# Kernel tuning notes

Measured on AMD Instinct MI355X. Metric: run time of the kernel, lower is better.

The kernel has to match this reference:

```python
import jax, jax.numpy as jnp
import numpy as np

T = 0.1  # temperature (init arg t)


def setup_inputs() -> dict:
    key = jax.random.key(0)
    k0, k1, k2, k3 = jax.random.split(key, 4)
    B, C, H, W, N = 1, 64, 256, 256, 4096
    emb_0 = jax.random.normal(k0, (B, C, H, W), dtype=jnp.float32)
    emb_1 = jax.random.normal(k1, (B, C, H, W), dtype=jnp.float32)
    # module assumes embeddings are already L2-normalized along channels
    emb_0 = emb_0 / jnp.linalg.norm(emb_0, axis=1, keepdims=True)
    emb_1 = emb_1 / jnp.linalg.norm(emb_1, axis=1, keepdims=True)
    locations_0 = jax.random.randint(k2, (B, N, 2), 0, H).astype(jnp.float32)
    locations_1 = jax.random.randint(k3, (B, N, 2), 0, H).astype(jnp.float32)
    return {"emb_0": emb_0, "emb_1": emb_1,
            "locations_0": locations_0, "locations_1": locations_1}


def reference(emb_0, emb_1, locations_0, locations_1):
    b, c, H, W = emb_0.shape  # b == 1
    n = locations_0.shape[1]
    v = H * W
    # (b, v, c)
    e0 = emb_0.reshape(b, c, v).transpose(0, 2, 1)
    e1 = emb_1.reshape(b, c, v).transpose(0, 2, 1)
    # flatten 2D coords to linear indices: strides [W, 1]
    ind_kernel = jnp.array([W, 1], dtype=jnp.float32)
    ind_0 = (jnp.floor(locations_0) @ ind_kernel).astype(jnp.int32)[0]  # (n,)
    ind_1 = (jnp.floor(locations_1) @ ind_kernel).astype(jnp.int32)[0]  # (n,)
    e0 = e0[:, ind_0, :]  # (b, n, c)
    e1 = e1[:, ind_1, :]  # (b, n, c)
    emb = jnp.concatenate([e0, e1], axis=1)  # (b, 2n, c)
    sim = jnp.einsum('bic,bjc->bij', emb, emb)  # (b, 2n, 2n)
    exp = jnp.exp(sim / T)
    sum_e = jnp.sum(exp, axis=2) - np.exp(1.0 / T)  # subtract self-similarity
    u = jnp.arange(n)
    w = u + n
    e_uv = exp[:, u, w]  # (b, n) positive pairs
    loss = -jnp.sum(jnp.log(e_uv / sum_e[:, u]) + jnp.log(e_uv / sum_e[:, w]))
    return loss / (2 * n)
```

## Files before the change

kernel.cpp:

```cpp
#include <hip/hip_runtime.h>
#include <math.h>

#define HW2     65536
#define NLOC    4096
#define NROW    8192
#define CDIM    64
#define TINV    10.0f
#define EXP10   22026.465794806718f
#define NP      64
#define NPAIR   2080

#if __has_builtin(__builtin_amdgcn_exp2f)
#define ASCALE  14.426950408889634f
#define EXPFN(x) __builtin_amdgcn_exp2f(x)
#else
#define ASCALE  10.0f
#define EXPFN(x) __expf(x)
#endif

typedef __attribute__((ext_vector_type(8))) short bf16x8;
typedef __attribute__((ext_vector_type(4))) float f32x4;
typedef unsigned short u16;

__device__ __forceinline__ unsigned short f2bf(float f) {
  unsigned u = __builtin_bit_cast(unsigned, f);
  u += 0x7FFFu + ((u >> 16) & 1u);
  return (unsigned short)(u >> 16);
}
__device__ __forceinline__ float bf2f(unsigned u16v) {
  unsigned u = u16v << 16;
  return __builtin_bit_cast(float, u);
}

__global__ __launch_bounds__(256) void transpose_kernel(
    const float* __restrict__ emb0, const float* __restrict__ emb1,
    u16* __restrict__ embT0, u16* __restrict__ embT1) {
  __shared__ u16 T[64 * 72];
  const int tid = threadIdx.x;
  const float* emb = blockIdx.y ? emb1 : emb0;
  u16* embT        = blockIdx.y ? embT1 : embT0;
  const int w0 = blockIdx.x * 64;

#pragma unroll
  for (int q = 0; q < 4; ++q) {
    const int c = q * 16 + (tid >> 4);
    const int x = tid & 15;
    float4 v = *reinterpret_cast<const float4*>(&emb[(size_t)c * HW2 + w0 + x * 4]);
    T[(x * 4 + 0) * 72 + c] = f2bf(v.x);
    T[(x * 4 + 1) * 72 + c] = f2bf(v.y);
    T[(x * 4 + 2) * 72 + c] = f2bf(v.z);
    T[(x * 4 + 3) * 72 + c] = f2bf(v.w);
  }
  __syncthreads();
#pragma unroll
  for (int q = 0; q < 2; ++q) {
    const int w  = q * 32 + (tid >> 3);
    const int c8 = tid & 7;
    bf16x8 v = *reinterpret_cast<const bf16x8*>(&T[w * 72 + c8 * 8]);
    *reinterpret_cast<bf16x8*>(&embT[(size_t)(w0 + w) * CDIM + c8 * 8]) = v;
  }
}

__global__ __launch_bounds__(256) void gather2_kernel(
    const u16* __restrict__ embT0, const u16* __restrict__ embT1,
    const float* __restrict__ loc0, const float* __restrict__ loc1,
    u16* __restrict__ Ga, u16* __restrict__ Gb) {
  const int t = blockIdx.x * 256 + threadIdx.x;
  const int i = t >> 3;
  const int p = t & 7;
  const float* loc = (i < NLOC) ? loc0 : loc1;
  const u16*   eT  = (i < NLOC) ? embT0 : embT1;
  const int u = (i < NLOC) ? i : i - NLOC;
  const int ind = (int)floorf(loc[u * 2]) * 256 + (int)floorf(loc[u * 2 + 1]);
  bf16x8 v = *reinterpret_cast<const bf16x8*>(&eT[(size_t)ind * CDIM + p * 8]);
  *reinterpret_cast<bf16x8*>(&Gb[(size_t)i * CDIM + p * 8]) = v;
  bf16x8 vs;
#pragma unroll
  for (int e = 0; e < 8; ++e) {
    float f = bf2f((unsigned short)v[e]);
    vs[e] = (short)f2bf(f * ASCALE);
  }
  *reinterpret_cast<bf16x8*>(&Ga[(size_t)i * CDIM + p * 8]) = vs;
}

__global__ __launch_bounds__(256) void gather_kernel(
    const float* __restrict__ emb0, const float* __restrict__ emb1,
    const float* __restrict__ loc0, const float* __restrict__ loc1,
    u16* __restrict__ Ga, u16* __restrict__ Gb) {
  int t = blockIdx.x * 256 + threadIdx.x;
  int i = t >> 6;
  int c = t & 63;
  const float* loc = (i < NLOC) ? loc0 : loc1;
  const float* emb = (i < NLOC) ? emb0 : emb1;
  int u = (i < NLOC) ? i : (i - NLOC);
  int ind = (int)floorf(loc[u * 2]) * 256 + (int)floorf(loc[u * 2 + 1]);
  float v = emb[(size_t)c * HW2 + ind];
  Gb[t] = f2bf(v);
  Ga[t] = f2bf(v * ASCALE);
}

__device__ __forceinline__ void stage_tile(u16* Bs, const u16* __restrict__ Gb,
                                           int jb, int buf, int tid, int wave,
                                           int srow, int ssl) {
#pragma unroll
  for (int r = 0; r < 2; ++r) {
    const u16* src = Gb + (size_t)(jb + r * 32 + srow) * CDIM + ssl * 8;
#if __has_builtin(__builtin_amdgcn_global_load_lds)
    u16* dst = Bs + buf * 4096 + r * 2048 + wave * 512;
    __builtin_amdgcn_global_load_lds(
        (const __attribute__((address_space(1))) unsigned int*)src,
        (__attribute__((address_space(3))) unsigned int*)dst, 16, 0, 0);
#else
    bf16x8 tmp = *reinterpret_cast<const bf16x8*>(src);
    *reinterpret_cast<bf16x8*>(Bs + buf * 4096 + r * 2048 + tid * 8) = tmp;
#endif
  }
}

__global__ __launch_bounds__(256) void simsum_tri_kernel(
    const u16* __restrict__ Ga, const u16* __restrict__ Gb,
    float* __restrict__ rowPart) {
  __shared__ u16 Bs[2 * 64 * CDIM];
  __shared__ float colRed[4][128];

  const int tid  = threadIdx.x;
  const int lane = tid & 63;
  const int wave = tid >> 6;
  const int lrow = lane & 15;
  const int kh   = lane >> 4;

  const int b = blockIdx.x;
  int p = (int)((129.0f - sqrtf(16641.0f - 8.0f * (float)b)) * 0.5f);
  if (p < 0) p = 0;
  if (p > NP - 1) p = NP - 1;
#pragma unroll
  for (int it = 0; it < 3; ++it) {
    if (p > 0 && (p * NP - p * (p - 1) / 2) > b) --p;
    else if (((p + 1) * NP - (p + 1) * p / 2) <= b) ++p;
  }
  const int q  = p + (b - (p * NP - p * (p - 1) / 2));
  const int p0 = p * 128, q0 = q * 128;
  const int i0 = p0 + wave * 32;

  const bf16x8* arowA =
      reinterpret_cast<const bf16x8*>(Ga + (size_t)(i0 + lrow) * CDIM + kh * 8);
  const bf16x8* arowB =
      reinterpret_cast<const bf16x8*>(Ga + (size_t)(i0 + 16 + lrow) * CDIM + kh * 8);
  bf16x8 aA0 = arowA[0], aA1 = arowA[4];
  bf16x8 aB0 = arowB[0], aB1 = arowB[4];

  const int srow = tid >> 3;
  const int ssl  = (tid & 7) ^ (srow & 7);
  stage_tile(Bs, Gb, q0,      0, tid, wave, srow, ssl);
  stage_tile(Bs, Gb, q0 + 64, 1, tid, wave, srow, ssl);
  __syncthreads();

  const int sp0 = ((kh ^ (lrow & 7)) << 3);
  const int sp1 = (((4 + kh) ^ (lrow & 7)) << 3);

  float accA[4][4], accB[4][4];
#pragma unroll
  for (int nf = 0; nf < 4; ++nf)
#pragma unroll
    for (int r = 0; r < 4; ++r) { accA[nf][r] = 0.f; accB[nf][r] = 0.f; }
  float colAcc[2][4];

#pragma unroll
  for (int t = 0; t < 2; ++t) {
    const u16* bs = Bs + t * 4096;
#pragma unroll
    for (int nf = 0; nf < 4; ++nf) {
      const int rb = (nf * 16 + lrow) * CDIM;
      bf16x8 b0 = *reinterpret_cast<const bf16x8*>(bs + rb + sp0);
      bf16x8 b1 = *reinterpret_cast<const bf16x8*>(bs + rb + sp1);
      f32x4 z = {0.f, 0.f, 0.f, 0.f};
      f32x4 tA = __builtin_amdgcn_mfma_f32_16x16x32_bf16(aA0, b0, z, 0, 0, 0);
      tA = __builtin_amdgcn_mfma_f32_16x16x32_bf16(aA1, b1, tA, 0, 0, 0);
      f32x4 tB = __builtin_amdgcn_mfma_f32_16x16x32_bf16(aB0, b0, z, 0, 0, 0);
      tB = __builtin_amdgcn_mfma_f32_16x16x32_bf16(aB1, b1, tB, 0, 0, 0);
      float cp = 0.f;
#pragma unroll
      for (int r = 0; r < 4; ++r) {
        float eA = EXPFN(tA[r]);
        float eB = EXPFN(tB[r]);
        accA[nf][r] += eA;
        accB[nf][r] += eB;
        cp += eA + eB;
      }
      colAcc[t][nf] = cp;
    }
  }

#pragma unroll
  for (int r = 0; r < 4; ++r) {
    float vA = (accA[0][r] + accA[1][r]) + (accA[2][r] + accA[3][r]);
    float vB = (accB[0][r] + accB[1][r]) + (accB[2][r] + accB[3][r]);
    vA += __shfl_xor(vA, 1, 16);
    vA += __shfl_xor(vA, 2, 16);
    vA += __shfl_xor(vA, 4, 16);
    vA += __shfl_xor(vA, 8, 16);
    vB += __shfl_xor(vB, 1, 16);
    vB += __shfl_xor(vB, 2, 16);
    vB += __shfl_xor(vB, 4, 16);
    vB += __shfl_xor(vB, 8, 16);
    if (lrow == 0) {
      rowPart[(size_t)(i0 + kh * 4 + r) * NP + q] = vA;
      rowPart[(size_t)(i0 + 16 + kh * 4 + r) * NP + q] = vB;
    }
  }

  if (p != q) {
#pragma unroll
    for (int t = 0; t < 2; ++t)
#pragma unroll
      for (int nf = 0; nf < 4; ++nf) {
        float c = colAcc[t][nf];
        c += __shfl_xor(c, 16, 64);
        c += __shfl_xor(c, 32, 64);
        if (kh == 0) colRed[wave][t * 64 + nf * 16 + lrow] = c;
      }
    __syncthreads();
    if (tid < 128) {
      float s = (colRed[0][tid] + colRed[1][tid]) +
                (colRed[2][tid] + colRed[3][tid]);
      rowPart[(size_t)(q0 + tid) * NP + p] = s;
    }
  }
}

__global__ __launch_bounds__(256) void finpart_kernel(
    const u16* __restrict__ Gb, const float* __restrict__ rowPart,
    float* __restrict__ partA, float* __restrict__ partB) {
  __shared__ float sA[256];
  __shared__ float sB[256];
  const int tid = threadIdx.x, b = blockIdx.x;

  float logAcc = 0.f;
  if (tid < 128) {
    const int row = b * 128 + tid;
    const float4* rp = reinterpret_cast<const float4*>(rowPart + (size_t)row * NP);
    float s = 0.f;
#pragma unroll
    for (int c = 0; c < NP / 4; ++c) {
      float4 v = rp[c];
      s += (v.x + v.y) + (v.z + v.w);
    }
    logAcc = logf(s - EXP10);
  }
  float cross = 0.f;
  if (tid < 64) {
    const int u = b * 64 + tid;
    const unsigned* r0 = reinterpret_cast<const unsigned*>(Gb + (size_t)u * CDIM);
    const unsigned* r1 =
        reinterpret_cast<const unsigned*>(Gb + (size_t)(u + NLOC) * CDIM);
#pragma unroll
    for (int c = 0; c < 32; ++c) {
      unsigned a = r0[c], bb = r1[c];
      cross += bf2f(a & 0xffffu) * bf2f(bb & 0xffffu) + bf2f(a >> 16) * bf2f(bb >> 16);
    }
  }
  sA[tid] = logAcc;
  sB[tid] = cross;
  __syncthreads();
  for (int s = 128; s > 0; s >>= 1) {
    if (tid < s) { sA[tid] += sA[tid + s]; sB[tid] += sB[tid + s]; }
    __syncthreads();
  }
  if (tid == 0) { partA[b] = sA[0]; partB[b] = sB[0]; }
}

__global__ __launch_bounds__(64) void fin2_kernel(
    const float* __restrict__ partA, const float* __restrict__ partB,
    float* __restrict__ out) {
  const int l = threadIdx.x;
  float a = partA[l];
  float c = partB[l];
#pragma unroll
  for (int s = 1; s < 64; s <<= 1) {
    a += __shfl_xor(a, s, 64);
    c += __shfl_xor(c, s, 64);
  }
  if (l == 0) out[0] = (a - 2.0f * TINV * c) / (float)NROW;
}

extern "C" void kernel_launch(void* const* d_in, const int* in_sizes, int n_in,
                              void* d_out, int out_size, void* d_ws, size_t ws_size,
                              hipStream_t stream) {
  const float* emb0 = (const float*)d_in[0];
  const float* emb1 = (const float*)d_in[1];
  const float* loc0 = (const float*)d_in[2];
  const float* loc1 = (const float*)d_in[3];
  float* out = (float*)d_out;
  char* ws = (char*)d_ws;

  const size_t NEED = (16ull << 20) + (2ull << 20) + (2ull << 20) + (8ull << 10);
  u16 *Ga, *Gb;
  float *rowPart, *partA, *partB;

  if (ws_size >= NEED) {
    u16* embT0 = (u16*)(ws);
    u16* embT1 = (u16*)(ws + (8ull << 20));
    Ga = (u16*)(ws + (16ull << 20));
    Gb = (u16*)(ws + (17ull << 20));
    rowPart = (float*)(ws + (18ull << 20));
    partA = (float*)(ws + (20ull << 20));
    partB = partA + 64;

    dim3 tg(HW2 / 64, 2);
    transpose_kernel<<<tg, 256, 0, stream>>>(emb0, emb1, embT0, embT1);
    gather2_kernel<<<(NROW * 8) / 256, 256, 0, stream>>>(embT0, embT1, loc0, loc1,
                                                         Ga, Gb);
  } else {
    Ga = (u16*)ws;
    Gb = Ga + (size_t)NROW * CDIM;
    rowPart = (float*)(Gb + (size_t)NROW * CDIM);
    partA = rowPart + (size_t)NROW * NP;
    partB = partA + 64;
    gather_kernel<<<(NROW * CDIM) / 256, 256, 0, stream>>>(emb0, emb1, loc0, loc1,
                                                           Ga, Gb);
  }

  simsum_tri_kernel<<<NPAIR, 256, 0, stream>>>(Ga, Gb, rowPart);
  finpart_kernel<<<64, 256, 0, stream>>>(Gb, rowPart, partA, partB);
  fin2_kernel<<<1, 64, 0, stream>>>(partA, partB, out);
}
```

Before: 38.52 us.

## Fuse transpose and gather into one kernel that scatters selected rows from LDS

Merges the full-image transpose and the separate gather into one kernel. Each block loads a 64-pixel window of channels into LDS, scans all 4096 locations to find the ones falling in its window, and writes only those rows to Ga/Gb. This removes the 16 MB bf16 transposed intermediate write and read plus one kernel launch. In exchange, every one of the 2048 blocks rereads the full location array and uses an LDS atomic counter. The whole embedding is still read once, and the fallback path for small workspaces is dropped.

```diff
diff --git a/kernel.cpp b/kernel.cpp
--- a/kernel.cpp
+++ b/kernel.cpp
@@ -32,14 +32,22 @@
   return __builtin_bit_cast(float, u);
 }
 
-__global__ __launch_bounds__(256) void transpose_kernel(
+__global__ __launch_bounds__(256) void tgather_kernel(
     const float* __restrict__ emb0, const float* __restrict__ emb1,
-    u16* __restrict__ embT0, u16* __restrict__ embT1) {
+    const float* __restrict__ loc0, const float* __restrict__ loc1,
+    u16* __restrict__ Ga, u16* __restrict__ Gb) {
   __shared__ u16 T[64 * 72];
+  __shared__ unsigned list[NLOC];
+  __shared__ unsigned nE;
+
   const int tid = threadIdx.x;
-  const float* emb = blockIdx.y ? emb1 : emb0;
-  u16* embT        = blockIdx.y ? embT1 : embT0;
-  const int w0 = blockIdx.x * 64;
+  const int win = blockIdx.x;
+  const int eb  = blockIdx.y;
+  const float* emb = eb ? emb1 : emb0;
+  const float* loc = eb ? loc1 : loc0;
+  const int w0 = win * 64;
+
+  if (tid == 0) nE = 0;
 
 #pragma unroll
   for (int q = 0; q < 4; ++q) {
@@ -52,35 +60,34 @@
     T[(x * 4 + 3) * 72 + c] = f2bf(v.w);
   }
   __syncthreads();
-#pragma unroll
-  for (int q = 0; q < 2; ++q) {
-    const int w  = q * 32 + (tid >> 3);
-    const int c8 = tid & 7;
+
+  for (int it = tid; it < NLOC; it += 256) {
+    float2 lv = *reinterpret_cast<const float2*>(&loc[it * 2]);
+    int ind = (int)floorf(lv.x) * 256 + (int)floorf(lv.y);
+    if ((ind >> 6) == win) {
+      unsigned slot = atomicAdd(&nE, 1u);
+      list[slot] = ((unsigned)it << 6) | (unsigned)(ind & 63);
+    }
+  }
+  __syncthreads();
+
+  const int n = (int)nE;
+  const int ibase = eb * NLOC;
+  const int c8 = tid & 7;
+  for (int s = (tid >> 3); s < n; s += 32) {
+    const unsigned ent = list[s];
+    const int i = (int)(ent >> 6) + ibase;
+    const int w = (int)(ent & 63u);
     bf16x8 v = *reinterpret_cast<const bf16x8*>(&T[w * 72 + c8 * 8]);
-    *reinterpret_cast<bf16x8*>(&embT[(size_t)(w0 + w) * CDIM + c8 * 8]) = v;
-  }
-}
-
-__global__ __launch_bounds__(256) void gather2_kernel(
-    const u16* __restrict__ embT0, const u16* __restrict__ embT1,
-    const float* __restrict__ loc0, const float* __restrict__ loc1,
-    u16* __restrict__ Ga, u16* __restrict__ Gb) {
-  const int t = blockIdx.x * 256 + threadIdx.x;
-  const int i = t >> 3;
-  const int p = t & 7;
-  const float* loc = (i < NLOC) ? loc0 : loc1;
-  const u16*   eT  = (i < NLOC) ? embT0 : embT1;
-  const int u = (i < NLOC) ? i : i - NLOC;
-  const int ind = (int)floorf(loc[u * 2]) * 256 + (int)floorf(loc[u * 2 + 1]);
-  bf16x8 v = *reinterpret_cast<const bf16x8*>(&eT[(size_t)ind * CDIM + p * 8]);
-  *reinterpret_cast<bf16x8*>(&Gb[(size_t)i * CDIM + p * 8]) = v;
-  bf16x8 vs;
-#pragma unroll
-  for (int e = 0; e < 8; ++e) {
-    float f = bf2f((unsigned short)v[e]);
-    vs[e] = (short)f2bf(f * ASCALE);
-  }
-  *reinterpret_cast<bf16x8*>(&Ga[(size_t)i * CDIM + p * 8]) = vs;
+    *reinterpret_cast<bf16x8*>(&Gb[(size_t)i * CDIM + c8 * 8]) = v;
+    bf16x8 vs;
+#pragma unroll
+    for (int j = 0; j < 8; ++j) {
+      float f = bf2f((unsigned short)v[j]);
+      vs[j] = (short)f2bf(f * ASCALE);
+    }
+    *reinterpret_cast<bf16x8*>(&Ga[(size_t)i * CDIM + c8 * 8]) = vs;
+  }
 }
 
 __global__ __launch_bounds__(256) void gather_kernel(
@@ -293,32 +300,14 @@
   float* out = (float*)d_out;
   char* ws = (char*)d_ws;
 
-  const size_t NEED = (16ull << 20) + (2ull << 20) + (2ull << 20) + (8ull << 10);
-  u16 *Ga, *Gb;
-  float *rowPart, *partA, *partB;
-
-  if (ws_size >= NEED) {
-    u16* embT0 = (u16*)(ws);
-    u16* embT1 = (u16*)(ws + (8ull << 20));
-    Ga = (u16*)(ws + (16ull << 20));
-    Gb = (u16*)(ws + (17ull << 20));
-    rowPart = (float*)(ws + (18ull << 20));
-    partA = (float*)(ws + (20ull << 20));
-    partB = partA + 64;
-
-    dim3 tg(HW2 / 64, 2);
-    transpose_kernel<<<tg, 256, 0, stream>>>(emb0, emb1, embT0, embT1);
-    gather2_kernel<<<(NROW * 8) / 256, 256, 0, stream>>>(embT0, embT1, loc0, loc1,
-                                                         Ga, Gb);
-  } else {
-    Ga = (u16*)ws;
-    Gb = Ga + (size_t)NROW * CDIM;
-    rowPart = (float*)(Gb + (size_t)NROW * CDIM);
-    partA = rowPart + (size_t)NROW * NP;
-    partB = partA + 64;
-    gather_kernel<<<(NROW * CDIM) / 256, 256, 0, stream>>>(emb0, emb1, loc0, loc1,
-                                                           Ga, Gb);
-  }
+  u16* Ga        = (u16*)ws;
+  u16* Gb        = (u16*)(ws + (1ull << 20));
+  float* rowPart = (float*)(ws + (2ull << 20));
+  float* partA   = (float*)(ws + (4ull << 20));
+  float* partB   = partA + 64;
+
+  dim3 tg(HW2 / 64, 2);
+  tgather_kernel<<<tg, 256, 0, stream>>>(emb0, emb1, loc0, loc1, Ga, Gb);
 
   simsum_tri_kernel<<<NPAIR, 256, 0, stream>>>(Ga, Gb, rowPart);
   finpart_kernel<<<64, 256, 0, stream>>>(Gb, rowPart, partA, partB);
```

Measured after the change: 41.46 us. 1.08x slower.
